# Kernel optimization log

Hardware: AMD Instinct MI355X
Metric: run time of the kernel (lower is better)

## Reference

```python
import jax, jax.numpy as jnp
import numpy as np

BIG = 1e9
GRAPH_LAYERS = 2
FLOW_ITERS = 10
DUAL_ITERS = 10
STEP = 0.1
MOM = 0.9


def _forward(node_features, node_embeddings, demands, adj, neighborhoods,
             enc_W0, enc_b0, enc_W1, enc_b1,
             attn_W, attn_a_src, attn_a_dst, nbr_q,
             gru_W, gru_U, gru_b,
             dec_W0, dec_b0, dec_W1, dec_b1,
             dual_W0, dual_b0, dual_W1, dual_b1):
    E = enc_W1.shape[1]
    K = neighborhoods.shape[0]
    # --- node encoder MLP (tanh, activate_final=True) ---
    x = jnp.concatenate([node_embeddings, node_features], axis=-1)  # [B,N,Fin]
    h = jnp.tanh(jnp.tanh(x @ enc_W0 + enc_b0) @ enc_W1 + enc_b1)   # [B,N,E]
    attn_coefs = None
    for _ in range(GRAPH_LAYERS):
        # --- AttentionNeighborhood: multi-head GAT per hop level, then attention over levels ---
        z = jnp.einsum('bnd,hde->hbne', h, attn_W)                   # [H,B,N,E]
        s_src = jnp.einsum('hbne,he->hbn', z, attn_a_src)
        s_dst = jnp.einsum('hbne,he->hbn', z, attn_a_dst)
        scores = jnp.tanh(s_src[:, :, :, None] + s_dst[:, :, None, :])  # [H,B,N,N]
        aggs = []
        for k in range(K):
            masked = jnp.where(neighborhoods[k][None] > 0, scores, -BIG)
            alpha = jax.nn.softmax(masked, axis=-1)                  # [H,B,N,N]
            agg = jnp.tanh(jnp.einsum('hbnm,hbme->hbne', alpha, z).mean(axis=0))  # heads averaged -> [B,N,E]
            aggs.append(agg)
        aggs = jnp.stack(aggs, axis=2)                               # [B,N,K,E]
        attn_coefs = jax.nn.softmax(jnp.tanh(jnp.einsum('bnke,e->bnk', aggs, nbr_q)), axis=-1)
        nxt = jnp.einsum('bnk,bnke->bne', attn_coefs, aggs)          # [B,N,E]
        # --- GRU state update (tanh activation) ---
        zr = jax.nn.sigmoid(nxt @ gru_W[:, :2 * E] + h @ gru_U[:, :2 * E] + gru_b[:2 * E])
        zg, r = zr[..., :E], zr[..., E:]
        h_tilde = jnp.tanh(nxt @ gru_W[:, 2 * E:] + (r * h) @ gru_U[:, 2 * E:] + gru_b[2 * E:])
        h = (1.0 - zg) * h + zg * h_tilde
    # --- flow-proportion decoder + masked softmax over neighbors ---
    node_weights = jnp.tanh(h @ dec_W0 + dec_b0) @ dec_W1 + dec_b1   # [B,N,1]
    pred = adj * jnp.swapaxes(node_weights, 1, 2)                    # adj * node_weights^T
    weights = -BIG * (1.0 - adj) + pred
    prop = jax.nn.softmax(weights, axis=-1)                          # [B,N,N]
    # --- iterative min-cost-flow solver ---
    def mcf_step(flow, _):
        inflow = flow.sum(axis=1)[:, :, None]                        # inflow_i = sum_j flow[j,i]
        return prop * jax.nn.relu(inflow - demands), None
    flow, _ = jax.lax.scan(mcf_step, jnp.zeros_like(prop), None, length=FLOW_ITERS)
    # should_correct_flows: cancel opposing flow on each edge pair
    flow = flow - adj * jnp.minimum(flow, jnp.swapaxes(flow, 1, 2))
    flow_cost = jnp.sum(flow * flow, axis=(1, 2))                    # square cost, per graph
    # --- dual decoder + projected momentum ascent dual-flow solver ---
    dual_vars = jnp.tanh(h @ dual_W0 + dual_b0) @ dual_W1 + dual_b1  # [B,N,1]
    dual_diff = adj * (dual_vars - jnp.swapaxes(dual_vars, 1, 2))    # [B,N,N]
    def dual_step(carry, _):
        y, m = carry
        g = 2.0 * y - dual_diff                                      # d/dy [y^2 - dual_diff*y]
        m = MOM * m + g
        y = adj * jax.nn.relu(y - STEP * m)
        return (y, m), None
    (dflow, _m), _ = jax.lax.scan(dual_step,
                                  (jnp.zeros_like(dual_diff), jnp.zeros_like(dual_diff)),
                                  None, length=DUAL_ITERS)
    dual_demand = jnp.sum(dual_vars * demands, axis=(1, 2))
    dual_cost = jnp.sum(dflow * dflow - dual_diff * dflow, axis=(1, 2)) - dual_demand
    return flow_cost - dual_cost                                     # primal-dual gap loss, [B]


def setup_inputs() -> dict:
    key = jax.random.key(0)
    ks = jax.random.split(key, 24)
    B, N, Femb, Ffeat, E, H = 2, 2048, 16, 2, 64, 2
    Fin = Femb + Ffeat
    node_embeddings = jax.random.normal(ks[0], (B, N, Femb), jnp.float32)
    node_features = jax.random.normal(ks[1], (B, N, Ffeat), jnp.float32)
    d = jax.random.normal(ks[2], (B, N, 1), jnp.float32) * 0.1
    demands = d - d.mean(axis=1, keepdims=True)                      # balanced demands
    eye = jnp.eye(N, dtype=jnp.float32)
    u = jax.random.uniform(ks[3], (B, N, N))
    adj = (u < 0.008).astype(jnp.float32) * (1.0 - eye)              # avg degree ~16
    a2 = (jnp.matmul(adj, adj) > 0).astype(jnp.float32) * (1.0 - eye)
    neighborhoods = jnp.stack([adj, a2], axis=0)                     # [K,B,N,N]
    def init(k, fan_in, shape):
        return jax.random.normal(k, shape, jnp.float32) / jnp.sqrt(float(fan_in))
    return {
        'node_features': node_features, 'node_embeddings': node_embeddings,
        'demands': demands, 'adj': adj, 'neighborhoods': neighborhoods,
        'enc_W0': init(ks[4], Fin, (Fin, 64)), 'enc_b0': jnp.zeros((64,)),
        'enc_W1': init(ks[5], 64, (64, E)), 'enc_b1': jnp.zeros((E,)),
        'attn_W': init(ks[6], E, (H, E, E)),
        'attn_a_src': init(ks[7], E, (H, E)), 'attn_a_dst': init(ks[8], E, (H, E)),
        'nbr_q': init(ks[9], E, (E,)),
        'gru_W': init(ks[10], E, (E, 3 * E)), 'gru_U': init(ks[11], E, (E, 3 * E)),
        'gru_b': jnp.zeros((3 * E,)),
        'dec_W0': init(ks[12], E, (E, 64)), 'dec_b0': jnp.zeros((64,)),
        'dec_W1': init(ks[13], 64, (64, 1)), 'dec_b1': jnp.zeros((1,)),
        'dual_W0': init(ks[14], E, (E, 64)), 'dual_b0': jnp.zeros((64,)),
        'dual_W1': init(ks[15], 64, (64, 1)), 'dual_b1': jnp.zeros((1,)),
    }


def reference(node_features, node_embeddings, demands, adj, neighborhoods,
              enc_W0, enc_b0, enc_W1, enc_b1,
              attn_W, attn_a_src, attn_a_dst, nbr_q,
              gru_W, gru_U, gru_b,
              dec_W0, dec_b0, dec_W1, dec_b1,
              dual_W0, dual_b0, dual_W1, dual_b1):
    return _forward(node_features, node_embeddings, demands, adj, neighborhoods,
                    enc_W0, enc_b0, enc_W1, enc_b1,
                    attn_W, attn_a_src, attn_a_dst, nbr_q,
                    gru_W, gru_U, gru_b,
                    dec_W0, dec_b0, dec_W1, dec_b1,
                    dual_W0, dual_b0, dual_W1, dual_b1)
```

## Files before the change

kernel.cpp:

```cpp
#include <hip/hip_runtime.h>

#define B_ 2
#define N_ 2048
#define E_ 64
#define FIN_ 18
#define ADJ_CAP 128
#define A2_CAP 1024
#define ROWS 8

__device__ __forceinline__ float wave_sum(float v) {
  #pragma unroll
  for (int o = 32; o > 0; o >>= 1) v += __shfl_xor(v, o);
  return v;
}
__device__ __forceinline__ float wave_max(float v) {
  #pragma unroll
  for (int o = 32; o > 0; o >>= 1) v = fmaxf(v, __shfl_xor(v, o));
  return v;
}
__device__ __forceinline__ void grp_reduce(float4& a) {
  #pragma unroll
  for (int o = 16; o <= 32; o <<= 1) {
    a.x += __shfl_xor(a.x, o); a.y += __shfl_xor(a.y, o);
    a.z += __shfl_xor(a.z, o); a.w += __shfl_xor(a.w, o);
  }
}

__global__ void k_csr(const float* __restrict__ nbhd, int* __restrict__ adj_idx,
                      int* __restrict__ adj_cnt, int* __restrict__ a2_idx,
                      int* __restrict__ a2_cnt, float* __restrict__ accum) {
  int wid = blockIdx.x * 4 + (threadIdx.x >> 6);
  int lane = threadIdx.x & 63;
  if (wid == 0 && lane < 8) accum[lane] = 0.f;
  int k = wid / (B_ * N_);
  int rem = wid - k * (B_ * N_);
  const float* row = nbhd + ((size_t)k * (B_ * N_) + rem) * N_;
  int cap = (k == 0) ? ADJ_CAP : A2_CAP;
  int* idx = ((k == 0) ? adj_idx : a2_idx) + (size_t)rem * cap;
  int* cntp = ((k == 0) ? adj_cnt : a2_cnt) + rem;
  int cnt = 0;
  unsigned long long below = (1ull << lane) - 1ull;
  for (int j0 = 0; j0 < N_; j0 += 256) {
    float4 v = ((const float4*)(row + j0))[lane];
    bool p0 = v.x > 0.f, p1 = v.y > 0.f, p2 = v.z > 0.f, p3 = v.w > 0.f;
    unsigned long long b0 = __ballot(p0), b1 = __ballot(p1),
                       b2 = __ballot(p2), b3 = __ballot(p3);
    int pos = cnt + __popcll(b0 & below) + __popcll(b1 & below) +
              __popcll(b2 & below) + __popcll(b3 & below);
    int base_j = j0 + lane * 4;
    if (p0) { if (pos < cap) idx[pos] = base_j;     pos++; }
    if (p1) { if (pos < cap) idx[pos] = base_j + 1; pos++; }
    if (p2) { if (pos < cap) idx[pos] = base_j + 2; pos++; }
    if (p3) { if (pos < cap) idx[pos] = base_j + 3; pos++; }
    cnt += __popcll(b0) + __popcll(b1) + __popcll(b2) + __popcll(b3);
  }
  if (lane == 0) *cntp = (cnt < cap) ? cnt : cap;
}

__global__ void k_enc(const float* __restrict__ emb, const float* __restrict__ feat,
                      const float* __restrict__ W0, const float* __restrict__ b0,
                      const float* __restrict__ W1, const float* __restrict__ b1,
                      float* __restrict__ h) {
  int j = threadIdx.x;
  int row0 = blockIdx.x * ROWS;
  __shared__ float X[ROWS][FIN_];
  __shared__ float HID[ROWS][64];
  for (int t = j; t < ROWS * FIN_; t += 64) {
    int r = t / FIN_, d = t % FIN_;
    int row = row0 + r;
    X[r][d] = (d < 16) ? emb[(size_t)row * 16 + d] : feat[(size_t)row * 2 + (d - 16)];
  }
  __syncthreads();
  float acc[ROWS];
  #pragma unroll
  for (int r = 0; r < ROWS; r++) acc[r] = b0[j];
  for (int d = 0; d < FIN_; d++) {
    float w = W0[d * 64 + j];
    #pragma unroll
    for (int r = 0; r < ROWS; r++) acc[r] += X[r][d] * w;
  }
  #pragma unroll
  for (int r = 0; r < ROWS; r++) HID[r][j] = tanhf(acc[r]);
  __syncthreads();
  float acc2[ROWS];
  #pragma unroll
  for (int r = 0; r < ROWS; r++) acc2[r] = b1[j];
  for (int d = 0; d < 64; d++) {
    float w = W1[d * 64 + j];
    #pragma unroll
    for (int r = 0; r < ROWS; r++) acc2[r] += HID[r][d] * w;
  }
  #pragma unroll
  for (int r = 0; r < ROWS; r++) h[(size_t)(row0 + r) * 64 + j] = tanhf(acc2[r]);
}

__global__ void k_z(const float* __restrict__ h, const float* __restrict__ attn_W,
                    const float* __restrict__ a_src, const float* __restrict__ a_dst,
                    float* __restrict__ z, float* __restrict__ ssrc2, float* __restrict__ sdst2) {
  int tid = threadIdx.x;
  int head = tid >> 6, j = tid & 63;
  int row0 = blockIdx.x * ROWS;
  __shared__ float HR[ROWS][64];
  for (int t = tid; t < ROWS * 64; t += 128) HR[t >> 6][t & 63] = h[(size_t)row0 * 64 + t];
  __syncthreads();
  float acc[ROWS];
  #pragma unroll
  for (int r = 0; r < ROWS; r++) acc[r] = 0.f;
  const float* W = attn_W + head * 64 * 64;
  for (int d = 0; d < 64; d++) {
    float w = W[d * 64 + j];
    #pragma unroll
    for (int r = 0; r < ROWS; r++) acc[r] += HR[r][d] * w;
  }
  float as = a_src[head * 64 + j], ad = a_dst[head * 64 + j];
  #pragma unroll
  for (int r = 0; r < ROWS; r++) {
    float zv = acc[r];
    z[((size_t)head * (B_ * N_) + row0 + r) * 64 + j] = zv;
    float rs = wave_sum(zv * as);
    float rd = wave_sum(zv * ad);
    if (j == 0) {
      ssrc2[(size_t)(row0 + r) * 2 + head] = rs;
      sdst2[(size_t)(row0 + r) * 2 + head] = rd;
    }
  }
}

__global__ __launch_bounds__(64) void k_agg_adj(
    const int* __restrict__ adj_idx, const int* __restrict__ adj_cnt,
    const float* __restrict__ z, const float* __restrict__ ssrc2,
    const float* __restrict__ sdst2, float* __restrict__ aggs) {
  int row = blockIdx.x;
  int lane = threadIdx.x;
  int b = row >> 11;
  int cnt = adj_cnt[row];
  const int* idx = adj_idx + (size_t)row * ADJ_CAP;
  float2 ss = ((const float2*)ssrc2)[row];
  const float2* sd = (const float2*)sdst2 + (size_t)b * N_;
  int col0 = 0, col1 = 0;
  float e00 = 0.f, e10 = 0.f, e01 = 0.f, e11 = 0.f;
  if (lane < cnt) {
    col0 = idx[lane]; float2 s = sd[col0];
    e00 = __expf(tanhf(ss.x + s.x)); e10 = __expf(tanhf(ss.y + s.y));
  }
  if (lane + 64 < cnt) {
    col1 = idx[lane + 64]; float2 s = sd[col1];
    e01 = __expf(tanhf(ss.x + s.x)); e11 = __expf(tanhf(ss.y + s.y));
  }
  float tot0 = wave_sum(e00 + e01), tot1 = wave_sum(e10 + e11);
  float inv0 = (tot0 > 0.f) ? 1.f / tot0 : 0.f;
  float inv1 = (tot1 > 0.f) ? 1.f / tot1 : 0.f;
  const float* z0 = z + (size_t)b * N_ * 64;
  const float* z1 = z + ((size_t)(B_ * N_) + b * N_) * 64;
  int g = lane >> 4, li = lane & 15;
  float4 a0 = {0.f, 0.f, 0.f, 0.f}, a1 = {0.f, 0.f, 0.f, 0.f};
  for (int j0 = 0; j0 < 64; j0 += 4) {
    if (j0 >= cnt) break;
    int j = j0 + g;
    int c = __shfl(col0, j);
    float e0 = __shfl(e00, j), e1 = __shfl(e10, j);
    if (j < cnt) {
      float4 v0 = ((const float4*)(z0 + (size_t)c * 64))[li];
      float4 v1 = ((const float4*)(z1 + (size_t)c * 64))[li];
      a0.x += e0 * v0.x; a0.y += e0 * v0.y; a0.z += e0 * v0.z; a0.w += e0 * v0.w;
      a1.x += e1 * v1.x; a1.y += e1 * v1.y; a1.z += e1 * v1.z; a1.w += e1 * v1.w;
    }
  }
  if (cnt > 64) {
    for (int j0 = 0; j0 < 64; j0 += 4) {
      if (64 + j0 >= cnt) break;
      int j = j0 + g;
      int c = __shfl(col1, j);
      float e0 = __shfl(e01, j), e1 = __shfl(e11, j);
      if (64 + j < cnt) {
        float4 v0 = ((const float4*)(z0 + (size_t)c * 64))[li];
        float4 v1 = ((const float4*)(z1 + (size_t)c * 64))[li];
        a0.x += e0 * v0.x; a0.y += e0 * v0.y; a0.z += e0 * v0.z; a0.w += e0 * v0.w;
        a1.x += e1 * v1.x; a1.y += e1 * v1.y; a1.z += e1 * v1.z; a1.w += e1 * v1.w;
      }
    }
  }
  grp_reduce(a0); grp_reduce(a1);
  if (g == 0) {
    float4 o;
    o.x = tanhf(0.5f * (a0.x * inv0 + a1.x * inv1));
    o.y = tanhf(0.5f * (a0.y * inv0 + a1.y * inv1));
    o.z = tanhf(0.5f * (a0.z * inv0 + a1.z * inv1));
    o.w = tanhf(0.5f * (a0.w * inv0 + a1.w * inv1));
    ((float4*)(aggs + ((size_t)row * 2 + 0) * 64))[li] = o;
  }
}

__global__ __launch_bounds__(256) void k_agg_a2(
    const int* __restrict__ a2_idx, const int* __restrict__ a2_cnt,
    const float* __restrict__ z, const float* __restrict__ ssrc2,
    const float* __restrict__ sdst2, float* __restrict__ aggs) {
  int row = blockIdx.x;
  int tid = threadIdx.x;
  int w = tid >> 6, lane = tid & 63;
  int b = row >> 11;
  int cnt = a2_cnt[row];
  const int* idx = a2_idx + (size_t)row * A2_CAP;
  float2 ss = ((const float2*)ssrc2)[row];
  const float2* sd = (const float2*)sdst2 + (size_t)b * N_;
  int colr[4]; float e0r[4], e1r[4];
  float s0 = 0.f, s1 = 0.f;
  #pragma unroll
  for (int c = 0; c < 4; c++) {
    int t = c * 256 + tid;
    colr[c] = 0; e0r[c] = 0.f; e1r[c] = 0.f;
    if (t < cnt) {
      int cc = idx[t]; colr[c] = cc;
      float2 s = sd[cc];
      e0r[c] = __expf(tanhf(ss.x + s.x));
      e1r[c] = __expf(tanhf(ss.y + s.y));
      s0 += e0r[c]; s1 += e1r[c];
    }
  }
  s0 = wave_sum(s0); s1 = wave_sum(s1);
  __shared__ float RED[2][4];
  __shared__ float WS0[4][64], WS1[4][64];
  if (lane == 0) { RED[0][w] = s0; RED[1][w] = s1; }
  const float* z0 = z + (size_t)b * N_ * 64;
  const float* z1 = z + ((size_t)(B_ * N_) + b * N_) * 64;
  int g = lane >> 4, li = lane & 15;
  float4 a0 = {0.f, 0.f, 0.f, 0.f}, a1 = {0.f, 0.f, 0.f, 0.f};
  #pragma unroll
  for (int c = 0; c < 4; c++) {
    int base = c * 256 + w * 64;
    if (base >= cnt) break;
    for (int j0 = 0; j0 < 64; j0 += 4) {
      if (base + j0 >= cnt) break;
      int j = j0 + g;
      int col = __shfl(colr[c], j);
      float e0 = __shfl(e0r[c], j), e1 = __shfl(e1r[c], j);
      if (base + j < cnt) {
        float4 v0 = ((const float4*)(z0 + (size_t)col * 64))[li];
        float4 v1 = ((const float4*)(z1 + (size_t)col * 64))[li];
        a0.x += e0 * v0.x; a0.y += e0 * v0.y; a0.z += e0 * v0.z; a0.w += e0 * v0.w;
        a1.x += e1 * v1.x; a1.y += e1 * v1.y; a1.z += e1 * v1.z; a1.w += e1 * v1.w;
      }
    }
  }
  grp_reduce(a0); grp_reduce(a1);
  if (g == 0) {
    ((float4*)WS0[w])[li] = a0;
    ((float4*)WS1[w])[li] = a1;
  }
  __syncthreads();
  if (tid < 64) {
    float tot0 = RED[0][0] + RED[0][1] + RED[0][2] + RED[0][3];
    float tot1 = RED[1][0] + RED[1][1] + RED[1][2] + RED[1][3];
    float inv0 = (tot0 > 0.f) ? 1.f / tot0 : 0.f;
    float inv1 = (tot1 > 0.f) ? 1.f / tot1 : 0.f;
    float r0 = WS0[0][tid] + WS0[1][tid] + WS0[2][tid] + WS0[3][tid];
    float r1 = WS1[0][tid] + WS1[1][tid] + WS1[2][tid] + WS1[3][tid];
    aggs[((size_t)row * 2 + 1) * 64 + tid] = tanhf(0.5f * (r0 * inv0 + r1 * inv1));
  }
}

__global__ void k_comb(const float* __restrict__ aggs, const float* __restrict__ nbr_q,
                       const float* __restrict__ gru_W, const float* __restrict__ gru_U,
                       const float* __restrict__ gru_b, float* __restrict__ h) {
  int tid = threadIdx.x;
  int w = tid >> 6, j = tid & 63;
  int row0 = blockIdx.x * ROWS;
  __shared__ float NXT[ROWS][64], HROW[ROWS][64], RG[ROWS][64], ZG[ROWS][64];
  for (int t = tid; t < ROWS * 64; t += 128) HROW[t >> 6][t & 63] = h[(size_t)row0 * 64 + t];
  float q = nbr_q[j];
  for (int r = w * (ROWS / 2); r < (w + 1) * (ROWS / 2); r++) {
    float a0 = aggs[((size_t)(row0 + r) * 2 + 0) * 64 + j];
    float a1 = aggs[((size_t)(row0 + r) * 2 + 1) * 64 + j];
    float t0 = tanhf(wave_sum(a0 * q));
    float t1 = tanhf(wave_sum(a1 * q));
    float mx = fmaxf(t0, t1);
    float e0 = __expf(t0 - mx), e1 = __expf(t1 - mx);
    float inv = 1.f / (e0 + e1);
    NXT[r][j] = (e0 * a0 + e1 * a1) * inv;
  }
  __syncthreads();
  {
    float acc[ROWS];
    #pragma unroll
    for (int r = 0; r < ROWS; r++) acc[r] = gru_b[tid];
    for (int d = 0; d < 64; d++) {
      float wW = gru_W[d * 192 + tid];
      float wU = gru_U[d * 192 + tid];
      #pragma unroll
      for (int r = 0; r < ROWS; r++) acc[r] += NXT[r][d] * wW + HROW[r][d] * wU;
    }
    #pragma unroll
    for (int r = 0; r < ROWS; r++) {
      float zr = 1.f / (1.f + __expf(-acc[r]));
      if (tid < 64) ZG[r][tid] = zr; else RG[r][tid - 64] = zr;
    }
  }
  __syncthreads();
  if (tid < 64) {
    int col = 128 + tid;
    float acc[ROWS];
    #pragma unroll
    for (int r = 0; r < ROWS; r++) acc[r] = gru_b[col];
    for (int d = 0; d < 64; d++) {
      float wW = gru_W[d * 192 + col];
      float wU = gru_U[d * 192 + col];
      #pragma unroll
      for (int r = 0; r < ROWS; r++) acc[r] += NXT[r][d] * wW + (RG[r][d] * HROW[r][d]) * wU;
    }
    #pragma unroll
    for (int r = 0; r < ROWS; r++) {
      float ht = tanhf(acc[r]);
      float zg = ZG[r][tid];
      h[(size_t)(row0 + r) * 64 + tid] = (1.f - zg) * HROW[r][tid] + zg * ht;
    }
  }
}

__global__ void k_dec(const float* __restrict__ h, const float* __restrict__ dW0,
                      const float* __restrict__ db0, const float* __restrict__ dW1,
                      const float* __restrict__ db1, const float* __restrict__ uW0,
                      const float* __restrict__ ub0, const float* __restrict__ uW1,
                      const float* __restrict__ ub1, const float* __restrict__ demands,
                      float* __restrict__ nw, float* __restrict__ dv, float* accum) {
  int j = threadIdx.x;
  int row0 = blockIdx.x * ROWS;
  __shared__ float HROW[ROWS][64];
  for (int t = j; t < ROWS * 64; t += 64) HROW[t >> 6][t & 63] = h[(size_t)row0 * 64 + t];
  __syncthreads();
  float hd[ROWS], hu[ROWS];
  #pragma unroll
  for (int r = 0; r < ROWS; r++) { hd[r] = db0[j]; hu[r] = ub0[j]; }
  for (int d = 0; d < 64; d++) {
    float w0 = dW0[d * 64 + j], u0 = uW0[d * 64 + j];
    #pragma unroll
    for (int r = 0; r < ROWS; r++) { hd[r] += HROW[r][d] * w0; hu[r] += HROW[r][d] * u0; }
  }
  float w1 = dW1[j], u1 = uW1[j];
  float ddl = 0.f;
  #pragma unroll
  for (int r = 0; r < ROWS; r++) {
    float a = wave_sum(tanhf(hd[r]) * w1);
    float bb = wave_sum(tanhf(hu[r]) * u1);
    if (j == 0) {
      int row = row0 + r;
      float nwv = a + db1[0], dvv = bb + ub1[0];
      nw[row] = nwv; dv[row] = dvv;
      ddl += dvv * demands[row];
    }
  }
  if (j == 0) atomicAdd(&accum[4 + (row0 >> 11)], ddl);
}

__global__ void k_prop(const int* __restrict__ adj_idx, const int* __restrict__ adj_cnt,
                       const float* __restrict__ nw, const float* __restrict__ demands,
                       float* __restrict__ Pval, float* __restrict__ sA,
                       int* __restrict__ tcnt) {
  int row = blockIdx.x;
  int lane = threadIdx.x;
  int b = row >> 11;
  int cnt = adj_cnt[row];
  const int* idx = adj_idx + (size_t)row * ADJ_CAP;
  int c0 = (lane < cnt) ? idx[lane] : -1;
  int c1 = (lane + 64 < cnt) ? idx[lane + 64] : -1;
  float v0 = (c0 >= 0) ? nw[b * N_ + c0] : -1e30f;
  float v1 = (c1 >= 0) ? nw[b * N_ + c1] : -1e30f;
  float m = wave_max(fmaxf(v0, v1));
  float e0 = (c0 >= 0) ? __expf(v0 - m) : 0.f;
  float e1 = (c1 >= 0) ? __expf(v1 - m) : 0.f;
  float s = wave_sum(e0 + e1);
  float inv = (s > 0.f) ? 1.f / s : 0.f;
  if (c0 >= 0) Pval[(size_t)row * ADJ_CAP + lane] = e0 * inv;
  if (c1 >= 0) Pval[(size_t)row * ADJ_CAP + lane + 64] = e1 * inv;
  if (lane == 0) sA[row] = fmaxf(-demands[row], 0.f);
  if (lane == 63) tcnt[row] = 0;
}

__global__ void k_transpose(const int* __restrict__ adj_idx, const int* __restrict__ adj_cnt,
                            const float* __restrict__ Pval, int* __restrict__ tcnt,
                            int* __restrict__ tsrc, float* __restrict__ tval) {
  int row = blockIdx.x;
  int lane = threadIdx.x;
  int cnt = adj_cnt[row];
  int base = row & ~(N_ - 1);
  for (int t = lane; t < cnt; t += 64) {
    int j = adj_idx[(size_t)row * ADJ_CAP + t];
    int col = base + j;
    int pos = atomicAdd(&tcnt[col], 1);
    if (pos < ADJ_CAP) {
      tsrc[(size_t)col * ADJ_CAP + pos] = row;
      tval[(size_t)col * ADJ_CAP + pos] = Pval[(size_t)row * ADJ_CAP + t];
    }
  }
}

__global__ void k_mcf_iter(const int* __restrict__ tcnt, const int* __restrict__ tsrc,
                           const float* __restrict__ tval, const float* __restrict__ demands,
                           const float* __restrict__ s_in, float* __restrict__ s_out) {
  int j = blockIdx.x * 64 + threadIdx.x;
  int cnt = tcnt[j];
  const int* src = tsrc + (size_t)j * ADJ_CAP;
  const float* val = tval + (size_t)j * ADJ_CAP;
  float c = 0.f;
  int c4 = cnt >> 2;
  for (int q = 0; q < c4; q++) {
    int4 s4 = ((const int4*)src)[q];
    float4 v4 = ((const float4*)val)[q];
    c += v4.x * s_in[s4.x] + v4.y * s_in[s4.y] + v4.z * s_in[s4.z] + v4.w * s_in[s4.w];
  }
  for (int t = c4 * 4; t < cnt; t++) c += val[t] * s_in[src[t]];
  s_out[j] = fmaxf(c - demands[j], 0.f);
}

__global__ __launch_bounds__(256) void k_flowdual(
    const int* __restrict__ adj_idx, const int* __restrict__ adj_cnt,
    const float* __restrict__ Pval, const float* __restrict__ s,
    const float* __restrict__ dv, float* accum) {
  int tid = threadIdx.x;
  int lane = tid & 63, w = tid >> 6;
  int r16 = lane >> 4, e = lane & 15;
  int row = blockIdx.x * 16 + w * 4 + r16;
  int b = row >> 11, i = row & (N_ - 1);
  int cnt = adj_cnt[row];
  float si = s[row], dvi = dv[row];
  const int* idx = adj_idx + (size_t)row * ADJ_CAP;
  const float* pv = Pval + (size_t)row * ADJ_CAP;
  float fc = 0.f, dc = 0.f;
  for (int t = e; t < cnt; t += 16) {
    int j = idx[t];
    float f_ij = si * pv[t];
    const int* jidx = adj_idx + (size_t)(b * N_ + j) * ADJ_CAP;
    int jcnt = adj_cnt[b * N_ + j];
    int lo = 0, hi = jcnt, pos = -1;
    while (lo < hi) {
      int mid = (lo + hi) >> 1;
      int v = jidx[mid];
      if (v == i) { pos = mid; break; }
      if (v < i) lo = mid + 1; else hi = mid;
    }
    float f_ji = (pos >= 0) ? s[b * N_ + j] * Pval[(size_t)(b * N_ + j) * ADJ_CAP + pos] : 0.f;
    float fin = f_ij - fminf(f_ij, f_ji);
    fc += fin * fin;
    float dd = dvi - dv[b * N_ + j];
    float y = 0.f, m = 0.f;
    #pragma unroll
    for (int q = 0; q < 10; q++) {
      float g = 2.f * y - dd;
      m = 0.9f * m + g;
      y = fmaxf(y - 0.1f * m, 0.f);
    }
    dc += y * y - dd * y;
  }
  fc = wave_sum(fc); dc = wave_sum(dc);
  __shared__ float FB[4], DB[4];
  if (lane == 0) { FB[w] = fc; DB[w] = dc; }
  __syncthreads();
  if (tid == 0) {
    int bb = (blockIdx.x * 16) >> 11;
    atomicAdd(&accum[bb], FB[0] + FB[1] + FB[2] + FB[3]);
    atomicAdd(&accum[2 + bb], DB[0] + DB[1] + DB[2] + DB[3]);
  }
}

__global__ void k_fin(const float* accum, float* out) {
  int b = threadIdx.x;
  if (b < B_) out[b] = accum[b] - accum[2 + b] + accum[4 + b];
}

extern "C" void kernel_launch(void* const* d_in, const int* in_sizes, int n_in,
                              void* d_out, int out_size, void* d_ws, size_t ws_size,
                              hipStream_t stream) {
  const float* feat    = (const float*)d_in[0];
  const float* emb     = (const float*)d_in[1];
  const float* demands = (const float*)d_in[2];
  const float* nbhd    = (const float*)d_in[4];
  const float* enc_W0  = (const float*)d_in[5];
  const float* enc_b0  = (const float*)d_in[6];
  const float* enc_W1  = (const float*)d_in[7];
  const float* enc_b1  = (const float*)d_in[8];
  const float* attn_W  = (const float*)d_in[9];
  const float* a_src   = (const float*)d_in[10];
  const float* a_dst   = (const float*)d_in[11];
  const float* nbr_q   = (const float*)d_in[12];
  const float* gru_W   = (const float*)d_in[13];
  const float* gru_U   = (const float*)d_in[14];
  const float* gru_b   = (const float*)d_in[15];
  const float* dec_W0  = (const float*)d_in[16];
  const float* dec_b0  = (const float*)d_in[17];
  const float* dec_W1  = (const float*)d_in[18];
  const float* dec_b1  = (const float*)d_in[19];
  const float* dual_W0 = (const float*)d_in[20];
  const float* dual_b0 = (const float*)d_in[21];
  const float* dual_W1 = (const float*)d_in[22];
  const float* dual_b1 = (const float*)d_in[23];
  float* out = (float*)d_out;

  char* ws = (char*)d_ws;
  size_t off = 0;
  auto alloc = [&](size_t bytes) { char* p = ws + off; off += (bytes + 255) & ~(size_t)255; return p; };
  int*   adj_idx = (int*)  alloc((size_t)B_ * N_ * ADJ_CAP * 4);
  int*   adj_cnt = (int*)  alloc((size_t)B_ * N_ * 4);
  int*   a2_idx  = (int*)  alloc((size_t)B_ * N_ * A2_CAP * 4);
  int*   a2_cnt  = (int*)  alloc((size_t)B_ * N_ * 4);
  float* h       = (float*)alloc((size_t)B_ * N_ * 64 * 4);
  float* z       = (float*)alloc((size_t)2 * B_ * N_ * 64 * 4);
  float* ssrc2   = (float*)alloc((size_t)2 * B_ * N_ * 4);
  float* sdst2   = (float*)alloc((size_t)2 * B_ * N_ * 4);
  float* aggs    = (float*)alloc((size_t)B_ * N_ * 2 * 64 * 4);
  float* nw      = (float*)alloc((size_t)B_ * N_ * 4);
  float* dv      = (float*)alloc((size_t)B_ * N_ * 4);
  float* Pval    = (float*)alloc((size_t)B_ * N_ * ADJ_CAP * 4);
  int*   tcnt    = (int*)  alloc((size_t)B_ * N_ * 4);
  int*   tsrc    = (int*)  alloc((size_t)B_ * N_ * ADJ_CAP * 4);
  float* tval    = (float*)alloc((size_t)B_ * N_ * ADJ_CAP * 4);
  float* sA      = (float*)alloc((size_t)B_ * N_ * 4);
  float* sB      = (float*)alloc((size_t)B_ * N_ * 4);
  float* accum   = (float*)alloc(8 * 4);

  k_csr<<<(2 * B_ * N_) / 4, 256, 0, stream>>>(nbhd, adj_idx, adj_cnt, a2_idx, a2_cnt, accum);
  k_enc<<<(B_ * N_) / ROWS, 64, 0, stream>>>(emb, feat, enc_W0, enc_b0, enc_W1, enc_b1, h);
  for (int layer = 0; layer < 2; layer++) {
    k_z<<<(B_ * N_) / ROWS, 128, 0, stream>>>(h, attn_W, a_src, a_dst, z, ssrc2, sdst2);
    k_agg_adj<<<B_ * N_, 64, 0, stream>>>(adj_idx, adj_cnt, z, ssrc2, sdst2, aggs);
    k_agg_a2<<<B_ * N_, 256, 0, stream>>>(a2_idx, a2_cnt, z, ssrc2, sdst2, aggs);
    k_comb<<<(B_ * N_) / ROWS, 128, 0, stream>>>(aggs, nbr_q, gru_W, gru_U, gru_b, h);
  }
  k_dec<<<(B_ * N_) / ROWS, 64, 0, stream>>>(h, dec_W0, dec_b0, dec_W1, dec_b1,
                                             dual_W0, dual_b0, dual_W1, dual_b1,
                                             demands, nw, dv, accum);
  k_prop<<<B_ * N_, 64, 0, stream>>>(adj_idx, adj_cnt, nw, demands, Pval, sA, tcnt);
  k_transpose<<<B_ * N_, 64, 0, stream>>>(adj_idx, adj_cnt, Pval, tcnt, tsrc, tval);
  for (int it = 0; it < 9; it++) {
    float* sin  = (it & 1) ? sB : sA;
    float* sout = (it & 1) ? sA : sB;
    k_mcf_iter<<<(B_ * N_) / 64, 64, 0, stream>>>(tcnt, tsrc, tval, demands, sin, sout);
  }
  k_flowdual<<<(B_ * N_) / 16, 256, 0, stream>>>(adj_idx, adj_cnt, Pval, sB, dv, accum);
  k_fin<<<1, 64, 0, stream>>>(accum, out);
}
```

Measured before the change: 416.3 us.

## Fuse MCF iterations into one persistent kernel and register-cache MLP weights

The nine per-iteration MCF launches become a single kernel per batch that keeps the state vectors and demands in shared memory and synchronises with block barriers. The dense encoder, attention-projection, GRU and decoder kernels now use 256-thread blocks over 16 rows, with weight columns preloaded into registers and float4 reads from shared memory. This targets launch overhead and redundant weight loads. The cost is that the MCF loop now runs on only two blocks, and the large per-thread register arrays may cause spills or lower occupancy.

```diff
diff --git a/kernel.cpp b/kernel.cpp
--- a/kernel.cpp
+++ b/kernel.cpp
@@ -6,7 +6,7 @@
 #define FIN_ 18
 #define ADJ_CAP 128
 #define A2_CAP 1024
-#define ROWS 8
+#define DR 16
 
 __device__ __forceinline__ float wave_sum(float v) {
   #pragma unroll
@@ -57,71 +57,81 @@
   if (lane == 0) *cntp = (cnt < cap) ? cnt : cap;
 }
 
-__global__ void k_enc(const float* __restrict__ emb, const float* __restrict__ feat,
-                      const float* __restrict__ W0, const float* __restrict__ b0,
-                      const float* __restrict__ W1, const float* __restrict__ b1,
-                      float* __restrict__ h) {
-  int j = threadIdx.x;
-  int row0 = blockIdx.x * ROWS;
-  __shared__ float X[ROWS][FIN_];
-  __shared__ float HID[ROWS][64];
-  for (int t = j; t < ROWS * FIN_; t += 64) {
-    int r = t / FIN_, d = t % FIN_;
+__global__ __launch_bounds__(256) void k_enc(
+    const float* __restrict__ emb, const float* __restrict__ feat,
+    const float* __restrict__ W0, const float* __restrict__ b0,
+    const float* __restrict__ W1, const float* __restrict__ b1,
+    float* __restrict__ h) {
+  int tid = threadIdx.x, w = tid >> 6, j = tid & 63;
+  int row0 = blockIdx.x * DR;
+  __shared__ float XL[DR][FIN_];
+  __shared__ float HID[DR][64];
+  for (int t = tid; t < DR * FIN_; t += 256) {
+    int r = t / FIN_, d = t - r * FIN_;
     int row = row0 + r;
-    X[r][d] = (d < 16) ? emb[(size_t)row * 16 + d] : feat[(size_t)row * 2 + (d - 16)];
-  }
-  __syncthreads();
-  float acc[ROWS];
-  #pragma unroll
-  for (int r = 0; r < ROWS; r++) acc[r] = b0[j];
-  for (int d = 0; d < FIN_; d++) {
-    float w = W0[d * 64 + j];
-    #pragma unroll
-    for (int r = 0; r < ROWS; r++) acc[r] += X[r][d] * w;
-  }
-  #pragma unroll
-  for (int r = 0; r < ROWS; r++) HID[r][j] = tanhf(acc[r]);
-  __syncthreads();
-  float acc2[ROWS];
-  #pragma unroll
-  for (int r = 0; r < ROWS; r++) acc2[r] = b1[j];
-  for (int d = 0; d < 64; d++) {
-    float w = W1[d * 64 + j];
-    #pragma unroll
-    for (int r = 0; r < ROWS; r++) acc2[r] += HID[r][d] * w;
-  }
-  #pragma unroll
-  for (int r = 0; r < ROWS; r++) h[(size_t)(row0 + r) * 64 + j] = tanhf(acc2[r]);
-}
-
-__global__ void k_z(const float* __restrict__ h, const float* __restrict__ attn_W,
-                    const float* __restrict__ a_src, const float* __restrict__ a_dst,
-                    float* __restrict__ z, float* __restrict__ ssrc2, float* __restrict__ sdst2) {
-  int tid = threadIdx.x;
-  int head = tid >> 6, j = tid & 63;
-  int row0 = blockIdx.x * ROWS;
-  __shared__ float HR[ROWS][64];
-  for (int t = tid; t < ROWS * 64; t += 128) HR[t >> 6][t & 63] = h[(size_t)row0 * 64 + t];
-  __syncthreads();
-  float acc[ROWS];
-  #pragma unroll
-  for (int r = 0; r < ROWS; r++) acc[r] = 0.f;
+    XL[r][d] = (d < 16) ? emb[(size_t)row * 16 + d] : feat[(size_t)row * 2 + (d - 16)];
+  }
+  float w0r[FIN_];
+  #pragma unroll
+  for (int d = 0; d < FIN_; d++) w0r[d] = W0[d * 64 + j];
+  float b0j = b0[j];
+  __syncthreads();
+  #pragma unroll
+  for (int r = 0; r < 4; r++) {
+    int rr = w * 4 + r;
+    float acc = b0j;
+    #pragma unroll
+    for (int d = 0; d < FIN_; d++) acc += XL[rr][d] * w0r[d];
+    HID[rr][j] = tanhf(acc);
+  }
+  float w1r[64];
+  #pragma unroll
+  for (int d = 0; d < 64; d++) w1r[d] = W1[d * 64 + j];
+  float b1j = b1[j];
+  #pragma unroll
+  for (int r = 0; r < 4; r++) {
+    int rr = w * 4 + r;
+    const float4* hv = (const float4*)HID[rr];
+    float acc = b1j;
+    #pragma unroll
+    for (int q = 0; q < 16; q++) {
+      float4 x = hv[q];
+      acc += x.x * w1r[4*q] + x.y * w1r[4*q+1] + x.z * w1r[4*q+2] + x.w * w1r[4*q+3];
+    }
+    h[(size_t)(row0 + rr) * 64 + j] = tanhf(acc);
+  }
+}
+
+__global__ __launch_bounds__(256) void k_z(
+    const float* __restrict__ h, const float* __restrict__ attn_W,
+    const float* __restrict__ a_src, const float* __restrict__ a_dst,
+    float* __restrict__ z, float* __restrict__ ssrc2, float* __restrict__ sdst2) {
+  int tid = threadIdx.x, w = tid >> 6, j = tid & 63;
+  int head = w & 1, rbase = (w >> 1) * 8;
+  int row0 = blockIdx.x * DR;
+  __shared__ float HL[DR][64];
+  for (int t = tid; t < DR * 64; t += 256) HL[t >> 6][t & 63] = h[(size_t)row0 * 64 + t];
+  float wr[64];
   const float* W = attn_W + head * 64 * 64;
-  for (int d = 0; d < 64; d++) {
-    float w = W[d * 64 + j];
-    #pragma unroll
-    for (int r = 0; r < ROWS; r++) acc[r] += HR[r][d] * w;
-  }
+  #pragma unroll
+  for (int d = 0; d < 64; d++) wr[d] = W[d * 64 + j];
   float as = a_src[head * 64 + j], ad = a_dst[head * 64 + j];
-  #pragma unroll
-  for (int r = 0; r < ROWS; r++) {
-    float zv = acc[r];
-    z[((size_t)head * (B_ * N_) + row0 + r) * 64 + j] = zv;
-    float rs = wave_sum(zv * as);
-    float rd = wave_sum(zv * ad);
+  __syncthreads();
+  for (int r = 0; r < 8; r++) {
+    int rr = rbase + r;
+    const float4* hv = (const float4*)HL[rr];
+    float acc = 0.f;
+    #pragma unroll
+    for (int q = 0; q < 16; q++) {
+      float4 x = hv[q];
+      acc += x.x * wr[4*q] + x.y * wr[4*q+1] + x.z * wr[4*q+2] + x.w * wr[4*q+3];
+    }
+    int row = row0 + rr;
+    z[((size_t)head * (B_ * N_) + row) * 64 + j] = acc;
+    float rs = wave_sum(acc * as), rd = wave_sum(acc * ad);
     if (j == 0) {
-      ssrc2[(size_t)(row0 + r) * 2 + head] = rs;
-      sdst2[(size_t)(row0 + r) * 2 + head] = rd;
+      ssrc2[(size_t)row * 2 + head] = rs;
+      sdst2[(size_t)row * 2 + head] = rd;
     }
   }
 }
@@ -259,101 +269,140 @@
   }
 }
 
-__global__ void k_comb(const float* __restrict__ aggs, const float* __restrict__ nbr_q,
-                       const float* __restrict__ gru_W, const float* __restrict__ gru_U,
-                       const float* __restrict__ gru_b, float* __restrict__ h) {
-  int tid = threadIdx.x;
-  int w = tid >> 6, j = tid & 63;
-  int row0 = blockIdx.x * ROWS;
-  __shared__ float NXT[ROWS][64], HROW[ROWS][64], RG[ROWS][64], ZG[ROWS][64];
-  for (int t = tid; t < ROWS * 64; t += 128) HROW[t >> 6][t & 63] = h[(size_t)row0 * 64 + t];
+__global__ __launch_bounds__(256) void k_comb(
+    const float* __restrict__ aggs, const float* __restrict__ nbr_q,
+    const float* __restrict__ gru_W, const float* __restrict__ gru_U,
+    const float* __restrict__ gru_b, float* __restrict__ h) {
+  int tid = threadIdx.x, w = tid >> 6, j = tid & 63;
+  int row0 = blockIdx.x * DR;
+  __shared__ float HL[DR][64], NL[DR][64], RGL[DR][64];
+  for (int t = tid; t < DR * 64; t += 256) HL[t >> 6][t & 63] = h[(size_t)row0 * 64 + t];
   float q = nbr_q[j];
-  for (int r = w * (ROWS / 2); r < (w + 1) * (ROWS / 2); r++) {
-    float a0 = aggs[((size_t)(row0 + r) * 2 + 0) * 64 + j];
-    float a1 = aggs[((size_t)(row0 + r) * 2 + 1) * 64 + j];
+  float zgr[4];
+  #pragma unroll
+  for (int r = 0; r < 4; r++) {
+    int rr = w * 4 + r, row = row0 + rr;
+    float a0 = aggs[((size_t)row * 2 + 0) * 64 + j];
+    float a1 = aggs[((size_t)row * 2 + 1) * 64 + j];
     float t0 = tanhf(wave_sum(a0 * q));
     float t1 = tanhf(wave_sum(a1 * q));
     float mx = fmaxf(t0, t1);
     float e0 = __expf(t0 - mx), e1 = __expf(t1 - mx);
     float inv = 1.f / (e0 + e1);
-    NXT[r][j] = (e0 * a0 + e1 * a1) * inv;
+    NL[rr][j] = (e0 * a0 + e1 * a1) * inv;
   }
   __syncthreads();
   {
-    float acc[ROWS];
-    #pragma unroll
-    for (int r = 0; r < ROWS; r++) acc[r] = gru_b[tid];
-    for (int d = 0; d < 64; d++) {
-      float wW = gru_W[d * 192 + tid];
-      float wU = gru_U[d * 192 + tid];
+    float gw[64], gu[64];
+    #pragma unroll
+    for (int d = 0; d < 64; d++) { gw[d] = gru_W[d * 192 + j]; gu[d] = gru_U[d * 192 + j]; }
+    float gb = gru_b[j];
+    #pragma unroll
+    for (int r = 0; r < 4; r++) {
+      int rr = w * 4 + r;
+      const float4* nv = (const float4*)NL[rr];
+      const float4* hv = (const float4*)HL[rr];
+      float acc = gb;
       #pragma unroll
-      for (int r = 0; r < ROWS; r++) acc[r] += NXT[r][d] * wW + HROW[r][d] * wU;
-    }
-    #pragma unroll
-    for (int r = 0; r < ROWS; r++) {
-      float zr = 1.f / (1.f + __expf(-acc[r]));
-      if (tid < 64) ZG[r][tid] = zr; else RG[r][tid - 64] = zr;
-    }
-  }
-  __syncthreads();
-  if (tid < 64) {
-    int col = 128 + tid;
-    float acc[ROWS];
-    #pragma unroll
-    for (int r = 0; r < ROWS; r++) acc[r] = gru_b[col];
-    for (int d = 0; d < 64; d++) {
-      float wW = gru_W[d * 192 + col];
-      float wU = gru_U[d * 192 + col];
+      for (int qd = 0; qd < 16; qd++) {
+        float4 n = nv[qd], hh = hv[qd];
+        acc += n.x * gw[4*qd] + n.y * gw[4*qd+1] + n.z * gw[4*qd+2] + n.w * gw[4*qd+3]
+             + hh.x * gu[4*qd] + hh.y * gu[4*qd+1] + hh.z * gu[4*qd+2] + hh.w * gu[4*qd+3];
+      }
+      zgr[r] = 1.f / (1.f + __expf(-acc));
+    }
+  }
+  {
+    float gw[64], gu[64];
+    #pragma unroll
+    for (int d = 0; d < 64; d++) { gw[d] = gru_W[d * 192 + 64 + j]; gu[d] = gru_U[d * 192 + 64 + j]; }
+    float gb = gru_b[64 + j];
+    #pragma unroll
+    for (int r = 0; r < 4; r++) {
+      int rr = w * 4 + r;
+      const float4* nv = (const float4*)NL[rr];
+      const float4* hv = (const float4*)HL[rr];
+      float acc = gb;
       #pragma unroll
-      for (int r = 0; r < ROWS; r++) acc[r] += NXT[r][d] * wW + (RG[r][d] * HROW[r][d]) * wU;
-    }
-    #pragma unroll
-    for (int r = 0; r < ROWS; r++) {
-      float ht = tanhf(acc[r]);
-      float zg = ZG[r][tid];
-      h[(size_t)(row0 + r) * 64 + tid] = (1.f - zg) * HROW[r][tid] + zg * ht;
-    }
-  }
-}
-
-__global__ void k_dec(const float* __restrict__ h, const float* __restrict__ dW0,
-                      const float* __restrict__ db0, const float* __restrict__ dW1,
-                      const float* __restrict__ db1, const float* __restrict__ uW0,
-                      const float* __restrict__ ub0, const float* __restrict__ uW1,
-                      const float* __restrict__ ub1, const float* __restrict__ demands,
-                      float* __restrict__ nw, float* __restrict__ dv, float* accum) {
-  int j = threadIdx.x;
-  int row0 = blockIdx.x * ROWS;
-  __shared__ float HROW[ROWS][64];
-  for (int t = j; t < ROWS * 64; t += 64) HROW[t >> 6][t & 63] = h[(size_t)row0 * 64 + t];
-  __syncthreads();
-  float hd[ROWS], hu[ROWS];
-  #pragma unroll
-  for (int r = 0; r < ROWS; r++) { hd[r] = db0[j]; hu[r] = ub0[j]; }
-  for (int d = 0; d < 64; d++) {
-    float w0 = dW0[d * 64 + j], u0 = uW0[d * 64 + j];
-    #pragma unroll
-    for (int r = 0; r < ROWS; r++) { hd[r] += HROW[r][d] * w0; hu[r] += HROW[r][d] * u0; }
-  }
-  float w1 = dW1[j], u1 = uW1[j];
+      for (int qd = 0; qd < 16; qd++) {
+        float4 n = nv[qd], hh = hv[qd];
+        acc += n.x * gw[4*qd] + n.y * gw[4*qd+1] + n.z * gw[4*qd+2] + n.w * gw[4*qd+3]
+             + hh.x * gu[4*qd] + hh.y * gu[4*qd+1] + hh.z * gu[4*qd+2] + hh.w * gu[4*qd+3];
+      }
+      RGL[rr][j] = 1.f / (1.f + __expf(-acc));
+    }
+  }
+  {
+    float gw[64], gu[64];
+    #pragma unroll
+    for (int d = 0; d < 64; d++) { gw[d] = gru_W[d * 192 + 128 + j]; gu[d] = gru_U[d * 192 + 128 + j]; }
+    float gb = gru_b[128 + j];
+    #pragma unroll
+    for (int r = 0; r < 4; r++) {
+      int rr = w * 4 + r;
+      const float4* nv = (const float4*)NL[rr];
+      const float4* hv = (const float4*)HL[rr];
+      const float4* rv = (const float4*)RGL[rr];
+      float acc = gb;
+      #pragma unroll
+      for (int qd = 0; qd < 16; qd++) {
+        float4 n = nv[qd], hh = hv[qd], rg = rv[qd];
+        acc += n.x * gw[4*qd] + n.y * gw[4*qd+1] + n.z * gw[4*qd+2] + n.w * gw[4*qd+3]
+             + rg.x * hh.x * gu[4*qd] + rg.y * hh.y * gu[4*qd+1]
+             + rg.z * hh.z * gu[4*qd+2] + rg.w * hh.w * gu[4*qd+3];
+      }
+      float ht = tanhf(acc);
+      float hj = HL[rr][j];
+      h[(size_t)(row0 + rr) * 64 + j] = (1.f - zgr[r]) * hj + zgr[r] * ht;
+    }
+  }
+}
+
+__global__ __launch_bounds__(256) void k_dec(
+    const float* __restrict__ h, const float* __restrict__ dW0,
+    const float* __restrict__ db0, const float* __restrict__ dW1,
+    const float* __restrict__ db1, const float* __restrict__ uW0,
+    const float* __restrict__ ub0, const float* __restrict__ uW1,
+    const float* __restrict__ ub1, const float* __restrict__ demands,
+    float* __restrict__ nw, float* __restrict__ dv, float* accum) {
+  int tid = threadIdx.x, w = tid >> 6, j = tid & 63;
+  int row0 = blockIdx.x * DR;
+  __shared__ float HL[DR][64];
+  __shared__ float DD[4];
+  for (int t = tid; t < DR * 64; t += 256) HL[t >> 6][t & 63] = h[(size_t)row0 * 64 + t];
+  float dw[64], uw[64];
+  #pragma unroll
+  for (int d = 0; d < 64; d++) { dw[d] = dW0[d * 64 + j]; uw[d] = uW0[d * 64 + j]; }
+  float db0j = db0[j], ub0j = ub0[j], dw1 = dW1[j], uw1 = uW1[j];
+  float db1s = db1[0], ub1s = ub1[0];
+  __syncthreads();
   float ddl = 0.f;
   #pragma unroll
-  for (int r = 0; r < ROWS; r++) {
-    float a = wave_sum(tanhf(hd[r]) * w1);
-    float bb = wave_sum(tanhf(hu[r]) * u1);
+  for (int r = 0; r < 4; r++) {
+    int rr = w * 4 + r, row = row0 + rr;
+    const float4* hv = (const float4*)HL[rr];
+    float accd = db0j, accu = ub0j;
+    #pragma unroll
+    for (int qd = 0; qd < 16; qd++) {
+      float4 hh = hv[qd];
+      accd += hh.x * dw[4*qd] + hh.y * dw[4*qd+1] + hh.z * dw[4*qd+2] + hh.w * dw[4*qd+3];
+      accu += hh.x * uw[4*qd] + hh.y * uw[4*qd+1] + hh.z * uw[4*qd+2] + hh.w * uw[4*qd+3];
+    }
+    float a = wave_sum(tanhf(accd) * dw1);
+    float bb = wave_sum(tanhf(accu) * uw1);
     if (j == 0) {
-      int row = row0 + r;
-      float nwv = a + db1[0], dvv = bb + ub1[0];
-      nw[row] = nwv; dv[row] = dvv;
+      float dvv = bb + ub1s;
+      nw[row] = a + db1s; dv[row] = dvv;
       ddl += dvv * demands[row];
     }
   }
-  if (j == 0) atomicAdd(&accum[4 + (row0 >> 11)], ddl);
+  if (j == 0) DD[w] = ddl;
+  __syncthreads();
+  if (tid == 0) atomicAdd(&accum[4 + (row0 >> 11)], DD[0] + DD[1] + DD[2] + DD[3]);
 }
 
 __global__ void k_prop(const int* __restrict__ adj_idx, const int* __restrict__ adj_cnt,
-                       const float* __restrict__ nw, const float* __restrict__ demands,
-                       float* __restrict__ Pval, float* __restrict__ sA,
+                       const float* __restrict__ nw, float* __restrict__ Pval,
                        int* __restrict__ tcnt) {
   int row = blockIdx.x;
   int lane = threadIdx.x;
@@ -371,8 +420,7 @@
   float inv = (s > 0.f) ? 1.f / s : 0.f;
   if (c0 >= 0) Pval[(size_t)row * ADJ_CAP + lane] = e0 * inv;
   if (c1 >= 0) Pval[(size_t)row * ADJ_CAP + lane + 64] = e1 * inv;
-  if (lane == 0) sA[row] = fmaxf(-demands[row], 0.f);
-  if (lane == 63) tcnt[row] = 0;
+  if (lane == 0) tcnt[row] = 0;
 }
 
 __global__ void k_transpose(const int* __restrict__ adj_idx, const int* __restrict__ adj_cnt,
@@ -393,22 +441,43 @@
   }
 }
 
-__global__ void k_mcf_iter(const int* __restrict__ tcnt, const int* __restrict__ tsrc,
-                           const float* __restrict__ tval, const float* __restrict__ demands,
-                           const float* __restrict__ s_in, float* __restrict__ s_out) {
-  int j = blockIdx.x * 64 + threadIdx.x;
-  int cnt = tcnt[j];
-  const int* src = tsrc + (size_t)j * ADJ_CAP;
-  const float* val = tval + (size_t)j * ADJ_CAP;
-  float c = 0.f;
-  int c4 = cnt >> 2;
-  for (int q = 0; q < c4; q++) {
-    int4 s4 = ((const int4*)src)[q];
-    float4 v4 = ((const float4*)val)[q];
-    c += v4.x * s_in[s4.x] + v4.y * s_in[s4.y] + v4.z * s_in[s4.z] + v4.w * s_in[s4.w];
-  }
-  for (int t = c4 * 4; t < cnt; t++) c += val[t] * s_in[src[t]];
-  s_out[j] = fmaxf(c - demands[j], 0.f);
+__global__ __launch_bounds__(1024) void k_mcf_all(
+    const int* __restrict__ tcnt, const int* __restrict__ tsrc,
+    const float* __restrict__ tval, const float* __restrict__ demands,
+    float* __restrict__ s_out) {
+  int b = blockIdx.x, tid = threadIdx.x;
+  __shared__ float SBUF[2][N_];
+  __shared__ float DL[N_];
+  for (int i = tid; i < N_; i += 1024) {
+    float d = demands[b * N_ + i];
+    DL[i] = d;
+    SBUF[0][i] = fmaxf(-d, 0.f);
+  }
+  __syncthreads();
+  int cur = 0;
+  for (int it = 0; it < 9; it++) {
+    const float* Sin = SBUF[cur];
+    float* Sout = SBUF[cur ^ 1];
+    for (int i = tid; i < N_; i += 1024) {
+      int gi = b * N_ + i;
+      int cnt = tcnt[gi];
+      const int* src = tsrc + (size_t)gi * ADJ_CAP;
+      const float* val = tval + (size_t)gi * ADJ_CAP;
+      float c = 0.f;
+      int c4 = cnt >> 2;
+      for (int qq = 0; qq < c4; qq++) {
+        int4 s4 = ((const int4*)src)[qq];
+        float4 v4 = ((const float4*)val)[qq];
+        c += v4.x * Sin[s4.x & (N_ - 1)] + v4.y * Sin[s4.y & (N_ - 1)]
+           + v4.z * Sin[s4.z & (N_ - 1)] + v4.w * Sin[s4.w & (N_ - 1)];
+      }
+      for (int t = c4 * 4; t < cnt; t++) c += val[t] * Sin[src[t] & (N_ - 1)];
+      Sout[i] = fmaxf(c - DL[i], 0.f);
+    }
+    __syncthreads();
+    cur ^= 1;
+  }
+  for (int i = tid; i < N_; i += 1024) s_out[b * N_ + i] = SBUF[cur][i];
 }
 
 __global__ __launch_bounds__(256) void k_flowdual(
@@ -512,28 +581,23 @@
   int*   tcnt    = (int*)  alloc((size_t)B_ * N_ * 4);
   int*   tsrc    = (int*)  alloc((size_t)B_ * N_ * ADJ_CAP * 4);
   float* tval    = (float*)alloc((size_t)B_ * N_ * ADJ_CAP * 4);
-  float* sA      = (float*)alloc((size_t)B_ * N_ * 4);
-  float* sB      = (float*)alloc((size_t)B_ * N_ * 4);
+  float* s_final = (float*)alloc((size_t)B_ * N_ * 4);
   float* accum   = (float*)alloc(8 * 4);
 
   k_csr<<<(2 * B_ * N_) / 4, 256, 0, stream>>>(nbhd, adj_idx, adj_cnt, a2_idx, a2_cnt, accum);
-  k_enc<<<(B_ * N_) / ROWS, 64, 0, stream>>>(emb, feat, enc_W0, enc_b0, enc_W1, enc_b1, h);
+  k_enc<<<(B_ * N_) / DR, 256, 0, stream>>>(emb, feat, enc_W0, enc_b0, enc_W1, enc_b1, h);
   for (int layer = 0; layer < 2; layer++) {
-    k_z<<<(B_ * N_) / ROWS, 128, 0, stream>>>(h, attn_W, a_src, a_dst, z, ssrc2, sdst2);
+    k_z<<<(B_ * N_) / DR, 256, 0, stream>>>(h, attn_W, a_src, a_dst, z, ssrc2, sdst2);
     k_agg_adj<<<B_ * N_, 64, 0, stream>>>(adj_idx, adj_cnt, z, ssrc2, sdst2, aggs);
     k_agg_a2<<<B_ * N_, 256, 0, stream>>>(a2_idx, a2_cnt, z, ssrc2, sdst2, aggs);
-    k_comb<<<(B_ * N_) / ROWS, 128, 0, stream>>>(aggs, nbr_q, gru_W, gru_U, gru_b, h);
-  }
-  k_dec<<<(B_ * N_) / ROWS, 64, 0, stream>>>(h, dec_W0, dec_b0, dec_W1, dec_b1,
-                                             dual_W0, dual_b0, dual_W1, dual_b1,
-                                             demands, nw, dv, accum);
-  k_prop<<<B_ * N_, 64, 0, stream>>>(adj_idx, adj_cnt, nw, demands, Pval, sA, tcnt);
+    k_comb<<<(B_ * N_) / DR, 256, 0, stream>>>(aggs, nbr_q, gru_W, gru_U, gru_b, h);
+  }
+  k_dec<<<(B_ * N_) / DR, 256, 0, stream>>>(h, dec_W0, dec_b0, dec_W1, dec_b1,
+                                            dual_W0, dual_b0, dual_W1, dual_b1,
+                                            demands, nw, dv, accum);
+  k_prop<<<B_ * N_, 64, 0, stream>>>(adj_idx, adj_cnt, nw, Pval, tcnt);
   k_transpose<<<B_ * N_, 64, 0, stream>>>(adj_idx, adj_cnt, Pval, tcnt, tsrc, tval);
-  for (int it = 0; it < 9; it++) {
-    float* sin  = (it & 1) ? sB : sA;
-    float* sout = (it & 1) ? sA : sB;
-    k_mcf_iter<<<(B_ * N_) / 64, 64, 0, stream>>>(tcnt, tsrc, tval, demands, sin, sout);
-  }
-  k_flowdual<<<(B_ * N_) / 16, 256, 0, stream>>>(adj_idx, adj_cnt, Pval, sB, dv, accum);
+  k_mcf_all<<<B_, 1024, 0, stream>>>(tcnt, tsrc, tval, demands, s_final);
+  k_flowdual<<<(B_ * N_) / 16, 256, 0, stream>>>(adj_idx, adj_cnt, Pval, s_final, dv, accum);
   k_fin<<<1, 64, 0, stream>>>(accum, out);
 }
```

Measured after the change: 596.8 us. +43.4%, slower.
